# Performance work log

Measured on AMD Instinct MI355X. Metric: run time of the kernel, lower is better.

The kernel has to match this reference:

```python
import jax, jax.numpy as jnp
import numpy as np

B, M, D = 16384, 32, 16
LAYERS = [64, 64, 64]


def setup_inputs() -> dict:
    key = jax.random.key(0)
    ks = jax.random.split(key, 4)
    inp = {"embeddings": jax.random.normal(ks[0], (B, M, D), dtype=jnp.float32)}
    hk_1 = M
    for i, hk in enumerate(LAYERS):
        # glorot-ish scale for W_i of shape (m, Hk_1, Hk)
        scale = (2.0 / (M * hk_1 + hk)) ** 0.5
        inp[f"W{i}"] = jax.random.normal(ks[i + 1], (M, hk_1, hk), dtype=jnp.float32) * scale
        hk_1 = hk
    return inp


def reference(embeddings, W0, W1, W2):
    # embeddings == x0: (B, m, D); W_i: (m, Hk_1, Hk)
    x0 = embeddings
    xk = x0  # x^{k-1}, starts as x0 with Hk_1 = m
    outs = []
    for W in (W0, W1, W2):
        # Fused form of: (x0[:,:,None,:] * xk[:,None,:,:])[..., None] * W -> sum over m, Hk_1
        # then permute to (B, Hk, D) and apply activation.
        xk = jax.nn.relu(jnp.einsum("bmd,bhd,mhk->bkd", x0, xk, W))  # (B, Hk, D)
        outs.append(jnp.sum(xk, axis=2))  # (B, Hk)
    return jnp.concatenate(outs, axis=1)  # (B, sum(layers_dim))
```

## Files before the change

### kernel.cpp

```cpp
#include <hip/hip_runtime.h>


typedef _Float16 half8 __attribute__((ext_vector_type(8)));
typedef _Float16 half4 __attribute__((ext_vector_type(4)));
typedef _Float16 half2v __attribute__((ext_vector_type(2)));
typedef float f32x4 __attribute__((ext_vector_type(4)));

#define OUT_STRIDE 192
#define X0B 512
#define XKR 72
#define XKB 1152

__global__ void prep_w_all(const float* __restrict__ W0,
                           const float* __restrict__ W1,
                           const float* __restrict__ W2,
                           _Float16* __restrict__ dst) {
  int e = blockIdx.x * 256 + threadIdx.x;
  const float* W;
  int logH, nkbLog, le;
  if (e < 65536)       { W = W0; logH = 5; nkbLog = 5; le = e; }
  else if (e < 196608) { W = W1; logH = 6; nkbLog = 6; le = e - 65536; }
  else                 { W = W2; logH = 6; nkbLog = 6; le = e - 196608; }
  int j    = le & 7;
  int lane = (le >> 3) & 63;
  int rr   = lane & 15, qq = lane >> 4;
  int rest = le >> 9;
  int kb   = rest & ((1 << nkbLog) - 1);
  int t    = rest >> nkbLog;
  int k    = kb * 32 + qq * 8 + j;
  int H    = 1 << logH;
  int m    = k >> logH, h = k & (H - 1);
  int n    = t * 16 + rr;
  dst[e] = (_Float16)W[(m * H + h) * 64 + n];
}

template<int NHI, bool LAST>
__device__ __forceinline__ void run_layer(
    const _Float16* __restrict__ Wp, const half8 (&av)[4][NHI],
    const _Float16* x0s, _Float16* xkw, float* __restrict__ out,
    long gb0, int loff, int lane, int r, int q)
{
  const int NKB = 32 * NHI;
  f32x4 acc[4][4];
#pragma unroll
  for (int b = 0; b < 4; ++b)
#pragma unroll
    for (int t = 0; t < 4; ++t) acc[b][t] = (f32x4){0.f, 0.f, 0.f, 0.f};

  const _Float16* Wl = Wp + lane * 8;

#pragma unroll 2
  for (int m = 0; m < 32; ++m) {
    half2v xs2[4];
#pragma unroll
    for (int b = 0; b < 4; ++b) {
      _Float16 x = x0s[b * X0B + m * 16 + r];
      xs2[b] = (half2v){x, x};
    }
#pragma unroll
    for (int hi = 0; hi < NHI; ++hi) {
      const int kb = m * NHI + hi;
      half8 Bf[4];
#pragma unroll
      for (int t = 0; t < 4; ++t)
        Bf[t] = *(const half8*)(Wl + (size_t)(t * NKB + kb) * 512);
#pragma unroll
      for (int b = 0; b < 4; ++b) {
        half8 af;
        half2v* ap = (half2v*)&af;
        const half2v* vp = (const half2v*)&av[b][hi];
#pragma unroll
        for (int j2 = 0; j2 < 4; ++j2) ap[j2] = vp[j2] * xs2[b];
#pragma unroll
        for (int t = 0; t < 4; ++t)
          acc[b][t] = __builtin_amdgcn_mfma_f32_16x16x32_f16(
              af, Bf[t], acc[b][t], 0, 0, 0);
      }
    }
  }

#pragma unroll
  for (int b = 0; b < 4; ++b) {
#pragma unroll
    for (int t = 0; t < 4; ++t) {
      float s = 0.f;
#pragma unroll
      for (int rr = 0; rr < 4; ++rr) {
        float v = acc[b][t][rr];
        v = v > 0.f ? v : 0.f;
        s += v;
        if (!LAST)
          xkw[b * XKB + (q * 4 + rr) * XKR + t * 16 + r] = (_Float16)v;
      }
      s += __shfl_xor(s, 16);
      s += __shfl_xor(s, 32);
      if (q == 0)
        out[(gb0 + b) * OUT_STRIDE + loff + t * 16 + r] = s;
    }
  }
}

__global__ __launch_bounds__(256, 3) void cin_main(
    const float* __restrict__ emb, const _Float16* __restrict__ Wall,
    float* __restrict__ out)
{
  __shared__ __align__(16) _Float16 lds[16 * X0B + 16 * XKB];
  const int lane = threadIdx.x & 63;
  const int wv = threadIdx.x >> 6;
  const int r = lane & 15, q = lane >> 4;
  const long gb0 = (long)blockIdx.x * 16 + wv * 4;

  _Float16* x0w = &lds[wv * 4 * X0B];
  _Float16* xkw = &lds[16 * X0B + wv * 4 * XKB];

#pragma unroll
  for (int bb = 0; bb < 4; ++bb) {
    const float* src = emb + (gb0 + bb) * 512;
    _Float16* dstb = x0w + bb * X0B;
#pragma unroll
    for (int i = 0; i < 2; ++i) {
      int f = i * 256 + lane * 4;
      float4 v = *(const float4*)(src + f);
      half4 h = {(_Float16)v.x, (_Float16)v.y, (_Float16)v.z, (_Float16)v.w};
      *(half4*)(dstb + f) = h;
    }
  }

  half8 av1[4][1];
#pragma unroll
  for (int b = 0; b < 4; ++b) {
#pragma unroll
    for (int j = 0; j < 8; ++j)
      av1[b][0][j] = x0w[b * X0B + (q * 8 + j) * 16 + r];
  }
  run_layer<1, false>(Wall, av1, x0w, xkw, out, gb0, 0, lane, r, q);

  half8 av2[4][2];
#pragma unroll
  for (int b = 0; b < 4; ++b)
#pragma unroll
    for (int hi = 0; hi < 2; ++hi)
      av2[b][hi] = *(const half8*)(xkw + b * XKB + r * XKR + hi * 32 + q * 8);
  run_layer<2, false>(Wall + 65536, av2, x0w, xkw, out, gb0, 64, lane, r, q);

#pragma unroll
  for (int b = 0; b < 4; ++b)
#pragma unroll
    for (int hi = 0; hi < 2; ++hi)
      av2[b][hi] = *(const half8*)(xkw + b * XKB + r * XKR + hi * 32 + q * 8);
  run_layer<2, true>(Wall + 196608, av2, x0w, xkw, out, gb0, 128, lane, r, q);
}

extern "C" void kernel_launch(void* const* d_in, const int* in_sizes, int n_in,
                              void* d_out, int out_size, void* d_ws, size_t ws_size,
                              hipStream_t stream) {
  const float* emb = (const float*)d_in[0];
  const float* W0  = (const float*)d_in[1];
  const float* W1  = (const float*)d_in[2];
  const float* W2  = (const float*)d_in[3];
  float* out = (float*)d_out;
  _Float16* ws = (_Float16*)d_ws;

  prep_w_all<<<1280, 256, 0, stream>>>(W0, W1, W2, ws);

  cin_main<<<1024, 256, 0, stream>>>(emb, ws, out);
}
```

Measured before the change: 207.1 us.

## Switch CIN layers from 16x16x32 to 32x32x16 MFMA tiles

Reorganises each wave's work so that two batch rows share the 32-row M dimension of a 32x32x16 f16 MFMA, with 32-wide output column tiles. The weight prep kernel is re-laid-out to match the new B-fragment shape, and the relu/sum epilogue is remapped to the 32x32 accumulator layout. The aim is fewer MFMA issues and fewer weight fragment loads per output, making better use of the matrix units. In exchange it uses larger accumulators (16 floats each), which raises register pressure, and it adds more complex index math in the epilogue.

```diff
diff --git a/kernel.cpp b/kernel.cpp
--- a/kernel.cpp
+++ b/kernel.cpp
@@ -4,7 +4,7 @@
 typedef _Float16 half8 __attribute__((ext_vector_type(8)));
 typedef _Float16 half4 __attribute__((ext_vector_type(4)));
 typedef _Float16 half2v __attribute__((ext_vector_type(2)));
-typedef float f32x4 __attribute__((ext_vector_type(4)));
+typedef float f32x16 __attribute__((ext_vector_type(16)));
 
 #define OUT_STRIDE 192
 #define X0B 512
@@ -18,84 +18,86 @@
   int e = blockIdx.x * 256 + threadIdx.x;
   const float* W;
   int logH, nkbLog, le;
-  if (e < 65536)       { W = W0; logH = 5; nkbLog = 5; le = e; }
-  else if (e < 196608) { W = W1; logH = 6; nkbLog = 6; le = e - 65536; }
-  else                 { W = W2; logH = 6; nkbLog = 6; le = e - 196608; }
+  if (e < 65536)       { W = W0; logH = 5; nkbLog = 6; le = e; }
+  else if (e < 196608) { W = W1; logH = 6; nkbLog = 7; le = e - 65536; }
+  else                 { W = W2; logH = 6; nkbLog = 7; le = e - 196608; }
   int j    = le & 7;
   int lane = (le >> 3) & 63;
-  int rr   = lane & 15, qq = lane >> 4;
   int rest = le >> 9;
   int kb   = rest & ((1 << nkbLog) - 1);
   int t    = rest >> nkbLog;
-  int k    = kb * 32 + qq * 8 + j;
+  int k    = kb * 16 + ((lane >> 5) << 3) + j;
   int H    = 1 << logH;
   int m    = k >> logH, h = k & (H - 1);
-  int n    = t * 16 + rr;
+  int n    = t * 32 + (lane & 31);
   dst[e] = (_Float16)W[(m * H + h) * 64 + n];
 }
 
-template<int NHI, bool LAST>
-__device__ __forceinline__ void run_layer(
-    const _Float16* __restrict__ Wp, const half8 (&av)[4][NHI],
+template<int NHB, bool LAST>
+__device__ __forceinline__ void run_layer32(
+    const _Float16* __restrict__ Wp, const half8 (&av)[2][NHB],
     const _Float16* x0s, _Float16* xkw, float* __restrict__ out,
-    long gb0, int loff, int lane, int r, int q)
+    long gb0, int loff, int lane, int dl, int pb, int kg)
 {
-  const int NKB = 32 * NHI;
-  f32x4 acc[4][4];
+  const int NKB = 32 * NHB;
+  f32x16 acc[2][2];
 #pragma unroll
-  for (int b = 0; b < 4; ++b)
+  for (int p = 0; p < 2; ++p)
 #pragma unroll
-    for (int t = 0; t < 4; ++t) acc[b][t] = (f32x4){0.f, 0.f, 0.f, 0.f};
+    for (int t = 0; t < 2; ++t)
+#pragma unroll
+      for (int rr = 0; rr < 16; ++rr) acc[p][t][rr] = 0.f;
 
   const _Float16* Wl = Wp + lane * 8;
+  const _Float16* x0l = x0s + pb * X0B + dl;
 
 #pragma unroll 2
   for (int m = 0; m < 32; ++m) {
-    half2v xs2[4];
+    half2v xs2[2];
 #pragma unroll
-    for (int b = 0; b < 4; ++b) {
-      _Float16 x = x0s[b * X0B + m * 16 + r];
-      xs2[b] = (half2v){x, x};
+    for (int p = 0; p < 2; ++p) {
+      _Float16 x = x0l[p * 2 * X0B + m * 16];
+      xs2[p] = (half2v){x, x};
     }
 #pragma unroll
-    for (int hi = 0; hi < NHI; ++hi) {
-      const int kb = m * NHI + hi;
-      half8 Bf[4];
+    for (int mh = 0; mh < NHB; ++mh) {
+      const int kb = m * NHB + mh;
+      half8 Bf0 = *(const half8*)(Wl + (size_t)(0 * NKB + kb) * 512);
+      half8 Bf1 = *(const half8*)(Wl + (size_t)(1 * NKB + kb) * 512);
 #pragma unroll
-      for (int t = 0; t < 4; ++t)
-        Bf[t] = *(const half8*)(Wl + (size_t)(t * NKB + kb) * 512);
-#pragma unroll
-      for (int b = 0; b < 4; ++b) {
+      for (int p = 0; p < 2; ++p) {
         half8 af;
         half2v* ap = (half2v*)&af;
-        const half2v* vp = (const half2v*)&av[b][hi];
+        const half2v* vp = (const half2v*)&av[p][mh];
 #pragma unroll
-        for (int j2 = 0; j2 < 4; ++j2) ap[j2] = vp[j2] * xs2[b];
-#pragma unroll
-        for (int t = 0; t < 4; ++t)
-          acc[b][t] = __builtin_amdgcn_mfma_f32_16x16x32_f16(
-              af, Bf[t], acc[b][t], 0, 0, 0);
+        for (int j2 = 0; j2 < 4; ++j2) ap[j2] = vp[j2] * xs2[p];
+        acc[p][0] = __builtin_amdgcn_mfma_f32_32x32x16_f16(af, Bf0, acc[p][0], 0, 0, 0);
+        acc[p][1] = __builtin_amdgcn_mfma_f32_32x32x16_f16(af, Bf1, acc[p][1], 0, 0, 0);
       }
     }
   }
 
 #pragma unroll
-  for (int b = 0; b < 4; ++b) {
+  for (int p = 0; p < 2; ++p) {
 #pragma unroll
-    for (int t = 0; t < 4; ++t) {
-      float s = 0.f;
+    for (int t = 0; t < 2; ++t) {
+      float s0 = 0.f, s1 = 0.f;
 #pragma unroll
-      for (int rr = 0; rr < 4; ++rr) {
-        float v = acc[b][t][rr];
+      for (int reg = 0; reg < 16; ++reg) {
+        float v = acc[p][t][reg];
         v = v > 0.f ? v : 0.f;
-        s += v;
+        const int pbq = reg >> 3;
+        const int d = (reg & 3) + 8 * ((reg >> 2) & 1) + 4 * kg;
         if (!LAST)
-          xkw[b * XKB + (q * 4 + rr) * XKR + t * 16 + r] = (_Float16)v;
+          xkw[(p * 2 + pbq) * XKB + d * XKR + t * 32 + (lane & 31)] = (_Float16)v;
+        if (pbq == 0) s0 += v; else s1 += v;
       }
-      s += __shfl_xor(s, 16);
-      s += __shfl_xor(s, 32);
-      if (q == 0)
-        out[(gb0 + b) * OUT_STRIDE + loff + t * 16 + r] = s;
+      s0 += __shfl_xor(s0, 32);
+      s1 += __shfl_xor(s1, 32);
+      if (kg == 0) {
+        out[(gb0 + p * 2 + 0) * OUT_STRIDE + loff + t * 32 + lane] = s0;
+        out[(gb0 + p * 2 + 1) * OUT_STRIDE + loff + t * 32 + lane] = s1;
+      }
     }
   }
 }
@@ -107,7 +109,9 @@
   __shared__ __align__(16) _Float16 lds[16 * X0B + 16 * XKB];
   const int lane = threadIdx.x & 63;
   const int wv = threadIdx.x >> 6;
-  const int r = lane & 15, q = lane >> 4;
+  const int dl = lane & 15;
+  const int pb = (lane >> 4) & 1;
+  const int kg = lane >> 5;
   const long gb0 = (long)blockIdx.x * 16 + wv * 4;
 
   _Float16* x0w = &lds[wv * 4 * X0B];
@@ -126,29 +130,33 @@
     }
   }
 
-  half8 av1[4][1];
+  half8 av1[2][2];
 #pragma unroll
-  for (int b = 0; b < 4; ++b) {
+  for (int p = 0; p < 2; ++p)
 #pragma unroll
-    for (int j = 0; j < 8; ++j)
-      av1[b][0][j] = x0w[b * X0B + (q * 8 + j) * 16 + r];
-  }
-  run_layer<1, false>(Wall, av1, x0w, xkw, out, gb0, 0, lane, r, q);
+    for (int mh = 0; mh < 2; ++mh)
+#pragma unroll
+      for (int j = 0; j < 8; ++j)
+        av1[p][mh][j] =
+            x0w[(p * 2 + pb) * X0B + (mh * 16 + kg * 8 + j) * 16 + dl];
+  run_layer32<2, false>(Wall, av1, x0w, xkw, out, gb0, 0, lane, dl, pb, kg);
 
-  half8 av2[4][2];
+  half8 av2[2][4];
 #pragma unroll
-  for (int b = 0; b < 4; ++b)
+  for (int p = 0; p < 2; ++p)
 #pragma unroll
-    for (int hi = 0; hi < 2; ++hi)
-      av2[b][hi] = *(const half8*)(xkw + b * XKB + r * XKR + hi * 32 + q * 8);
-  run_layer<2, false>(Wall + 65536, av2, x0w, xkw, out, gb0, 64, lane, r, q);
+    for (int mh = 0; mh < 4; ++mh)
+      av2[p][mh] = *(const half8*)(xkw + (p * 2 + pb) * XKB + dl * XKR +
+                                   mh * 16 + kg * 8);
+  run_layer32<4, false>(Wall + 65536, av2, x0w, xkw, out, gb0, 64, lane, dl, pb, kg);
 
 #pragma unroll
-  for (int b = 0; b < 4; ++b)
+  for (int p = 0; p < 2; ++p)
 #pragma unroll
-    for (int hi = 0; hi < 2; ++hi)
-      av2[b][hi] = *(const half8*)(xkw + b * XKB + r * XKR + hi * 32 + q * 8);
-  run_layer<2, true>(Wall + 196608, av2, x0w, xkw, out, gb0, 128, lane, r, q);
+    for (int mh = 0; mh < 4; ++mh)
+      av2[p][mh] = *(const half8*)(xkw + (p * 2 + pb) * XKB + dl * XKR +
+                                   mh * 16 + kg * 8);
+  run_layer32<4, true>(Wall + 196608, av2, x0w, xkw, out, gb0, 128, lane, dl, pb, kg);
 }
 
 extern "C" void kernel_launch(void* const* d_in, const int* in_sizes, int n_in,
```

After: 226.5 us. 1.09x slower.

## Transpose x0 in LDS, pair m-steps, and vectorize weight prep reads

Applied to the files above, without the earlier changes.

The x0 tile in shared memory is stored transposed (d-major with padded row stride 34), so each lane fetches two consecutive m values with a single half2 load. The m loop is restructured into pairs handled by a helper with unroll 1. The weight-prep kernel now reads float4 coalesced from the source and scatters to the swizzled fp16 layout using a quarter of the threads. Together these aim to cut LDS load count, bank conflicts and global read inefficiency in prep, at the cost of scattered 2-byte LDS and global writes.

```diff
diff --git a/kernel.cpp b/kernel.cpp
--- a/kernel.cpp
+++ b/kernel.cpp
@@ -7,7 +7,8 @@
 typedef float f32x4 __attribute__((ext_vector_type(4)));
 
 #define OUT_STRIDE 192
-#define X0B 512
+#define X0R 34
+#define X0B 544
 #define XKR 72
 #define XKB 1152
 
@@ -15,23 +16,53 @@
                            const float* __restrict__ W1,
                            const float* __restrict__ W2,
                            _Float16* __restrict__ dst) {
-  int e = blockIdx.x * 256 + threadIdx.x;
+  int g = blockIdx.x * 256 + threadIdx.x;
   const float* W;
-  int logH, nkbLog, le;
-  if (e < 65536)       { W = W0; logH = 5; nkbLog = 5; le = e; }
-  else if (e < 196608) { W = W1; logH = 6; nkbLog = 6; le = e - 65536; }
-  else                 { W = W2; logH = 6; nkbLog = 6; le = e - 196608; }
-  int j    = le & 7;
-  int lane = (le >> 3) & 63;
-  int rr   = lane & 15, qq = lane >> 4;
-  int rest = le >> 9;
-  int kb   = rest & ((1 << nkbLog) - 1);
-  int t    = rest >> nkbLog;
-  int k    = kb * 32 + qq * 8 + j;
-  int H    = 1 << logH;
-  int m    = k >> logH, h = k & (H - 1);
-  int n    = t * 16 + rr;
-  dst[e] = (_Float16)W[(m * H + h) * 64 + n];
+  int nkb, dbase, lg;
+  if (g < 16384)      { W = W0; nkb = 32; dbase = 0;      lg = g; }
+  else if (g < 49152) { W = W1; nkb = 64; dbase = 65536;  lg = g - 16384; }
+  else                { W = W2; nkb = 64; dbase = 196608; lg = g - 49152; }
+  int s  = lg * 4;
+  int k  = s >> 6;
+  int n0 = s & 63;
+  float4 v = *(const float4*)(W + s);
+  int kb = k >> 5, qq = (k >> 3) & 3, j = k & 7;
+  float vv[4] = {v.x, v.y, v.z, v.w};
+#pragma unroll
+  for (int i = 0; i < 4; ++i) {
+    int n = n0 + i;
+    int t = n >> 4, rr = n & 15;
+    int lane = qq * 16 + rr;
+    dst[dbase + (((t * nkb + kb) * 64 + lane) << 3) + j] = (_Float16)vv[i];
+  }
+}
+
+template<int NHI>
+__device__ __forceinline__ void do_group(
+    const _Float16* __restrict__ Wl, const half8 (&av)[4][NHI],
+    const half2v (&xs2)[4], f32x4 (&acc)[4][4], int m)
+{
+  const int NKB = 32 * NHI;
+#pragma unroll
+  for (int hi = 0; hi < NHI; ++hi) {
+    const int kb = m * NHI + hi;
+    half8 Bf[4];
+#pragma unroll
+    for (int t = 0; t < 4; ++t)
+      Bf[t] = *(const half8*)(Wl + (size_t)(t * NKB + kb) * 512);
+#pragma unroll
+    for (int b = 0; b < 4; ++b) {
+      half8 af;
+      half2v* ap = (half2v*)&af;
+      const half2v* vp = (const half2v*)&av[b][hi];
+#pragma unroll
+      for (int j2 = 0; j2 < 4; ++j2) ap[j2] = vp[j2] * xs2[b];
+#pragma unroll
+      for (int t = 0; t < 4; ++t)
+        acc[b][t] = __builtin_amdgcn_mfma_f32_16x16x32_f16(
+            af, Bf[t], acc[b][t], 0, 0, 0);
+    }
+  }
 }
 
 template<int NHI, bool LAST>
@@ -40,7 +71,6 @@
     const _Float16* x0s, _Float16* xkw, float* __restrict__ out,
     long gb0, int loff, int lane, int r, int q)
 {
-  const int NKB = 32 * NHI;
   f32x4 acc[4][4];
 #pragma unroll
   for (int b = 0; b < 4; ++b)
@@ -48,35 +78,19 @@
     for (int t = 0; t < 4; ++t) acc[b][t] = (f32x4){0.f, 0.f, 0.f, 0.f};
 
   const _Float16* Wl = Wp + lane * 8;
+  const _Float16* x0l = x0s + r * X0R;
 
-#pragma unroll 2
-  for (int m = 0; m < 32; ++m) {
-    half2v xs2[4];
+#pragma unroll 1
+  for (int mp = 0; mp < 16; ++mp) {
+    half2v xsl[4], xsh[4];
 #pragma unroll
     for (int b = 0; b < 4; ++b) {
-      _Float16 x = x0s[b * X0B + m * 16 + r];
-      xs2[b] = (half2v){x, x};
+      half2v p = *(const half2v*)(x0l + b * X0B + 2 * mp);
+      xsl[b] = (half2v){p.x, p.x};
+      xsh[b] = (half2v){p.y, p.y};
     }
-#pragma unroll
-    for (int hi = 0; hi < NHI; ++hi) {
-      const int kb = m * NHI + hi;
-      half8 Bf[4];
-#pragma unroll
-      for (int t = 0; t < 4; ++t)
-        Bf[t] = *(const half8*)(Wl + (size_t)(t * NKB + kb) * 512);
-#pragma unroll
-      for (int b = 0; b < 4; ++b) {
-        half8 af;
-        half2v* ap = (half2v*)&af;
-        const half2v* vp = (const half2v*)&av[b][hi];
-#pragma unroll
-        for (int j2 = 0; j2 < 4; ++j2) ap[j2] = vp[j2] * xs2[b];
-#pragma unroll
-        for (int t = 0; t < 4; ++t)
-          acc[b][t] = __builtin_amdgcn_mfma_f32_16x16x32_f16(
-              af, Bf[t], acc[b][t], 0, 0, 0);
-      }
-    }
+    do_group<NHI>(Wl, av, xsl, acc, 2 * mp);
+    do_group<NHI>(Wl, av, xsh, acc, 2 * mp + 1);
   }
 
 #pragma unroll
@@ -121,8 +135,11 @@
     for (int i = 0; i < 2; ++i) {
       int f = i * 256 + lane * 4;
       float4 v = *(const float4*)(src + f);
-      half4 h = {(_Float16)v.x, (_Float16)v.y, (_Float16)v.z, (_Float16)v.w};
-      *(half4*)(dstb + f) = h;
+      int m = f >> 4, d = f & 15;
+      dstb[(d + 0) * X0R + m] = (_Float16)v.x;
+      dstb[(d + 1) * X0R + m] = (_Float16)v.y;
+      dstb[(d + 2) * X0R + m] = (_Float16)v.z;
+      dstb[(d + 3) * X0R + m] = (_Float16)v.w;
     }
   }
 
@@ -131,7 +148,7 @@
   for (int b = 0; b < 4; ++b) {
 #pragma unroll
     for (int j = 0; j < 8; ++j)
-      av1[b][0][j] = x0w[b * X0B + (q * 8 + j) * 16 + r];
+      av1[b][0][j] = x0w[b * X0B + r * X0R + q * 8 + j];
   }
   run_layer<1, false>(Wall, av1, x0w, xkw, out, gb0, 0, lane, r, q);
 
@@ -161,7 +178,7 @@
   float* out = (float*)d_out;
   _Float16* ws = (_Float16*)d_ws;
 
-  prep_w_all<<<1280, 256, 0, stream>>>(W0, W1, W2, ws);
+  prep_w_all<<<320, 256, 0, stream>>>(W0, W1, W2, ws);
 
   cin_main<<<1024, 256, 0, stream>>>(emb, ws, out);
 }
```

Result: no change. 207.7 us (+0.3%).
